# Optimization experiments

Measured on AMD Instinct MI355X. Metric: run time of the kernel, lower is better.

## Reference

```python
import jax, jax.numpy as jnp
import numpy as np

IN_DIM = 1024
QK_DIM = 64
NHEADS = 12
HN_MULT = 4
BATCH = 2
SEQ = 2048
BETA = 1.0 / np.sqrt(QK_DIM)


def setup_inputs() -> dict:
    key = jax.random.key(0)
    kg, kq, kk, kw = jax.random.split(key, 4)
    scale = 1.0 / np.sqrt(IN_DIM)
    g = jax.random.normal(kg, (BATCH, SEQ, IN_DIM), dtype=jnp.float32)
    Wq = jax.random.normal(kq, (NHEADS, QK_DIM, IN_DIM), dtype=jnp.float32) * scale
    Wk = jax.random.normal(kk, (NHEADS, QK_DIM, IN_DIM), dtype=jnp.float32) * scale
    Whn = jax.random.normal(kw, (HN_MULT * IN_DIM, IN_DIM), dtype=jnp.float32) * scale
    return {"g": g, "Wq": Wq, "Wk": Wk, "Whn": Whn}


def reference(g, Wq, Wk, Whn):
    # --- attention energy (Energy Transformer): E = -(1/beta) * sum logsumexp_keys(beta * q.k)
    q = jnp.einsum("bnd,hkd->bhnk", g, Wq)  # [B,H,N,K]
    k = jnp.einsum("bnd,hkd->bhnk", g, Wk)  # [B,H,N,K]
    scores = BETA * jnp.einsum("bhnk,bhmk->bhnm", q, k)  # [B,H,N(query),M(key)]
    e_attn = -(1.0 / BETA) * jnp.sum(jax.nn.logsumexp(scores, axis=-1))
    # --- Hopfield energy: -0.5 * sum(relu(W g)^2)
    h = jnp.einsum("bnd,md->bnm", g, Whn)  # [B,N,4*D]
    e_hn = -0.5 * jnp.sum(jax.nn.relu(h) ** 2)
    return e_attn + e_hn
```

## Files before the change

kernel.cpp:

```cpp
#include <hip/hip_runtime.h>
#include <hip/hip_bf16.h>

typedef __attribute__((ext_vector_type(4))) float f32x4;
typedef __attribute__((ext_vector_type(8))) short bf16x8;
typedef unsigned short u16;
typedef __attribute__((ext_vector_type(4))) u16 u16x4;


#define OFF_GB    ((size_t)0)
#define OFF_WQB   ((size_t)8388608)
#define OFF_WKB   ((size_t)(8388608+1572864))
#define OFF_WHNB  ((size_t)(8388608+2*1572864))
#define OFF_QB    (OFF_WHNB + 8388608)
#define OFF_KB    (OFF_QB + 6291456)
#define OFF_ROWSUM (OFF_KB + 6291456)

__device__ __forceinline__ u16 f2bf(float f) {
  union { float f; unsigned u; } x; x.f = f;
  unsigned u = x.u;
  u += 0x7fffu + ((u >> 16) & 1u);
  return (u16)(u >> 16);
}

__global__ __launch_bounds__(256) void convert_all(
    const float* __restrict__ g, const float* __restrict__ wq,
    const float* __restrict__ wk, const float* __restrict__ whn,
    u16* __restrict__ gB, u16* __restrict__ wqB, u16* __restrict__ wkB, u16* __restrict__ whnB)
{
  const int NG = 1048576;
  const int NW = 196608;
  const int total = NG + 2 * NW + NG;
  for (int i = blockIdx.x * blockDim.x + threadIdx.x; i < total; i += gridDim.x * blockDim.x) {
    const float4* src; u16* dst; int j; float scale = 1.0f;
    if (i < NG)              { src = (const float4*)g;   dst = gB;   j = i; }
    else if (i < NG + NW)    { src = (const float4*)wq;  dst = wqB;  j = i - NG;
                               scale = 0.125f * 1.44269504089f; }
    else if (i < NG + 2*NW)  { src = (const float4*)wk;  dst = wkB;  j = i - NG - NW; }
    else                     { src = (const float4*)whn; dst = whnB; j = i - NG - 2*NW; }
    float4 v = src[j];
    u16x4 o;
    o.x = f2bf(v.x * scale); o.y = f2bf(v.y * scale);
    o.z = f2bf(v.z * scale); o.w = f2bf(v.w * scale);
    *(u16x4*)(dst + (size_t)j * 4) = o;
  }
}

__global__ __launch_bounds__(256) void gemm_bt(
    const u16* __restrict__ A, const u16* __restrict__ B0, const u16* __restrict__ B1,
    u16* __restrict__ C0, u16* __restrict__ C1, int K)
{
  __shared__ u16 lA[128 * 64];
  __shared__ u16 lB[128 * 64];
  const int tid = threadIdx.x;
  const int lane = tid & 63;
  const int w = tid >> 6;
  const int bid = blockIdx.x;
  const int xcd = bid & 7, idx = bid >> 3;
  const int bm = ((xcd >> 1) << 3) + (idx & 7);
  const int bn = (xcd & 1) * 6 + (idx >> 3);

  const u16* Bp; u16* Cp; int bcol0;
  if (bn < 6) { Bp = B0; Cp = C0; bcol0 = bn * 128; }
  else        { Bp = B1; Cp = C1; bcol0 = (bn - 6) * 128; }
  const int arow0 = bm * 128;
  const int wr = w >> 1, wc = w & 1;
  const int l15 = lane & 15, lg = lane >> 4;

  f32x4 acc[4][4];
  const f32x4 zz = {0.f, 0.f, 0.f, 0.f};
#pragma unroll
  for (int m = 0; m < 4; m++)
#pragma unroll
    for (int n = 0; n < 4; n++) acc[m][n] = zz;

#define STAGE(KT) do {                                                                     \
    _Pragma("unroll")                                                                      \
    for (int i = 0; i < 4; i++) {                                                          \
      int rloc = w * 32 + i * 8 + (lane >> 3);                                             \
      int cb   = (((lane & 7) ^ (rloc & 7)) << 4);                                         \
      const char* srcA = (const char*)A + (((size_t)(arow0 + rloc)) * K + (KT) * 64) * 2 + cb; \
      __builtin_amdgcn_global_load_lds((const __attribute__((address_space(1))) void*)srcA, \
          (__attribute__((address_space(3))) void*)((char*)lA + (w * 32 + i * 8) * 128), 16, 0, 0); \
      const char* srcB = (const char*)Bp + (((size_t)(bcol0 + rloc)) * K + (KT) * 64) * 2 + cb; \
      __builtin_amdgcn_global_load_lds((const __attribute__((address_space(1))) void*)srcB, \
          (__attribute__((address_space(3))) void*)((char*)lB + (w * 32 + i * 8) * 128), 16, 0, 0); \
    }                                                                                      \
  } while (0)

  STAGE(0);
  const int nkt = K / 64;
  for (int kt = 0; kt < nkt; ++kt) {
    __syncthreads();
    bf16x8 a0[4], a1[4], b0[4], b1[4];
#pragma unroll
    for (int m = 0; m < 4; m++) {
      int row = wr * 64 + m * 16 + l15;
      const char* base = (const char*)lA + row * 128;
      int sw = (row & 7) << 4;
      a0[m] = *(const bf16x8*)(base + ((lg * 16) ^ sw));
      a1[m] = *(const bf16x8*)(base + ((64 + lg * 16) ^ sw));
    }
#pragma unroll
    for (int n = 0; n < 4; n++) {
      int row = wc * 64 + n * 16 + l15;
      const char* base = (const char*)lB + row * 128;
      int sw = (row & 7) << 4;
      b0[n] = *(const bf16x8*)(base + ((lg * 16) ^ sw));
      b1[n] = *(const bf16x8*)(base + ((64 + lg * 16) ^ sw));
    }
    __syncthreads();
    if (kt + 1 < nkt) STAGE(kt + 1);
#pragma unroll
    for (int m = 0; m < 4; m++)
#pragma unroll
      for (int n = 0; n < 4; n++) {
        acc[m][n] = __builtin_amdgcn_mfma_f32_16x16x32_bf16(a0[m], b0[n], acc[m][n], 0, 0, 0);
        acc[m][n] = __builtin_amdgcn_mfma_f32_16x16x32_bf16(a1[m], b1[n], acc[m][n], 0, 0, 0);
      }
  }
#pragma unroll
  for (int m = 0; m < 4; m++)
#pragma unroll
    for (int n = 0; n < 4; n++)
#pragma unroll
      for (int r = 0; r < 4; r++) {
        int row = arow0 + wr * 64 + m * 16 + lg * 4 + r;
        int col = bcol0 + wc * 64 + n * 16 + l15;
        size_t dst = ((((size_t)(row >> 11) * 12 + (col >> 6)) << 11) + (row & 2047)) * 64 + (col & 63);
        Cp[dst] = f2bf(acc[m][n][r]);
      }
#undef STAGE
}

__global__ __launch_bounds__(512, 2) void hop_gemm8(
    const u16* __restrict__ A, const u16* __restrict__ Bm, float* __restrict__ out)
{
  __shared__ __align__(16) u16 lds[2][2][2][128][64];
  const int tid = threadIdx.x;
  const int lane = tid & 63, w = tid >> 6;
  const int wr = w >> 2, wc = w & 3;
  const int l15 = lane & 15, lg = lane >> 4;
  const int bid = blockIdx.x;
  const int xcd = bid & 7, idx = bid >> 3;
  const int am0 = (((xcd >> 1) << 2) + (idx & 3)) * 256;
  const int bn0 = (((xcd & 1) << 3) + (idx >> 2)) * 256;
  constexpr int nkt = 16;

  f32x4 acc[8][4];
  const f32x4 zz = {0.f, 0.f, 0.f, 0.f};
#pragma unroll
  for (int i = 0; i < 8; i++)
#pragma unroll
    for (int j = 0; j < 4; j++) acc[i][j] = zz;

#define HSTAGE(KT, MAT, H) do {                                                            \
    const u16* s_ = (MAT) ? Bm : A;                                                        \
    int rb_ = ((MAT) ? bn0 : am0) + (H) * 128;                                             \
    char* d0_ = (char*)&lds[(KT) & 1][(MAT)][(H)][0][0];                                   \
    _Pragma("unroll")                                                                      \
    for (int q_ = 0; q_ < 2; q_++) {                                                       \
      int r_ = q_ * 64 + (tid >> 3);                                                       \
      int cb_ = ((tid & 7) * 16) ^ ((r_ & 7) << 4);                                        \
      const char* g_ = (const char*)s_ + (size_t)(rb_ + r_) * 2048 + (KT) * 128 + cb_;     \
      __builtin_amdgcn_global_load_lds((const __attribute__((address_space(1))) void*)g_,  \
          (__attribute__((address_space(3))) void*)(d0_ + q_ * 8192 + tid * 16), 16, 0, 0);\
    }                                                                                      \
  } while (0)

#define LDA_F(DST, P, I, S) do {                                                           \
    int rh_ = ((I) & 3) * 32 + wr * 16 + l15;                                              \
    const char* b_ = (const char*)&lds[(P)][0][(I) >> 2][0][0] + rh_ * 128;                \
    DST = *(const bf16x8*)(b_ + (((S) * 64 + lg * 16) ^ ((rh_ & 7) << 4)));                \
  } while (0)
#define LDB_F(DST, P, J, S) do {                                                           \
    int rh_ = ((J) & 1) * 64 + wc * 16 + l15;                                              \
    const char* b_ = (const char*)&lds[(P)][1][(J) >> 1][0][0] + rh_ * 128;                \
    DST = *(const bf16x8*)(b_ + (((S) * 64 + lg * 16) ^ ((rh_ & 7) << 4)));                \
  } while (0)

  HSTAGE(0, 0, 0); HSTAGE(0, 1, 0); HSTAGE(0, 1, 1); HSTAGE(0, 0, 1);
  HSTAGE(1, 0, 0); HSTAGE(1, 1, 0); HSTAGE(1, 1, 1);
  asm volatile("s_waitcnt vmcnt(6)" ::: "memory");
  __builtin_amdgcn_s_barrier();

  bf16x8 af[4][2], bf[4][2];

#pragma unroll 2
  for (int t = 0; t < nkt; ++t) {
    const int p = t & 1;
#pragma unroll
    for (int m = 0; m < 4; m++) { LDA_F(af[m][0], p, m, 0); LDA_F(af[m][1], p, m, 1); }
#pragma unroll
    for (int n = 0; n < 2; n++) { LDB_F(bf[n][0], p, n, 0); LDB_F(bf[n][1], p, n, 1); }
    if (t + 1 < nkt) HSTAGE(t + 1, 0, 1);
    __builtin_amdgcn_s_barrier();
    __builtin_amdgcn_s_setprio(1);
#pragma unroll
    for (int m = 0; m < 4; m++)
#pragma unroll
      for (int n = 0; n < 2; n++) {
        acc[m][n] = __builtin_amdgcn_mfma_f32_16x16x32_bf16(af[m][0], bf[n][0], acc[m][n], 0, 0, 0);
        acc[m][n] = __builtin_amdgcn_mfma_f32_16x16x32_bf16(af[m][1], bf[n][1], acc[m][n], 0, 0, 0);
      }
    __builtin_amdgcn_s_setprio(0);
    __builtin_amdgcn_s_barrier();
#pragma unroll
    for (int n = 2; n < 4; n++) { LDB_F(bf[n][0], p, n, 0); LDB_F(bf[n][1], p, n, 1); }
    if (t + 2 < nkt) HSTAGE(t + 2, 0, 0);
    __builtin_amdgcn_s_barrier();
    __builtin_amdgcn_s_setprio(1);
#pragma unroll
    for (int m = 0; m < 4; m++)
#pragma unroll
      for (int n = 2; n < 4; n++) {
        acc[m][n] = __builtin_amdgcn_mfma_f32_16x16x32_bf16(af[m][0], bf[n][0], acc[m][n], 0, 0, 0);
        acc[m][n] = __builtin_amdgcn_mfma_f32_16x16x32_bf16(af[m][1], bf[n][1], acc[m][n], 0, 0, 0);
      }
    __builtin_amdgcn_s_setprio(0);
    __builtin_amdgcn_s_barrier();
#pragma unroll
    for (int m = 0; m < 4; m++) { LDA_F(af[m][0], p, m + 4, 0); LDA_F(af[m][1], p, m + 4, 1); }
    if (t + 2 < nkt) HSTAGE(t + 2, 1, 0);
    __builtin_amdgcn_s_barrier();
    __builtin_amdgcn_s_setprio(1);
#pragma unroll
    for (int m = 0; m < 4; m++)
#pragma unroll
      for (int n = 2; n < 4; n++) {
        acc[m + 4][n] = __builtin_amdgcn_mfma_f32_16x16x32_bf16(af[m][0], bf[n][0], acc[m + 4][n], 0, 0, 0);
        acc[m + 4][n] = __builtin_amdgcn_mfma_f32_16x16x32_bf16(af[m][1], bf[n][1], acc[m + 4][n], 0, 0, 0);
      }
    __builtin_amdgcn_s_setprio(0);
    __builtin_amdgcn_s_barrier();
    if (t + 2 < nkt) HSTAGE(t + 2, 1, 1);
    __builtin_amdgcn_s_barrier();
    __builtin_amdgcn_s_setprio(1);
#pragma unroll
    for (int m = 0; m < 4; m++)
#pragma unroll
      for (int n = 0; n < 2; n++) {
        acc[m + 4][n] = __builtin_amdgcn_mfma_f32_16x16x32_bf16(af[m][0], bf[n][0], acc[m + 4][n], 0, 0, 0);
        acc[m + 4][n] = __builtin_amdgcn_mfma_f32_16x16x32_bf16(af[m][1], bf[n][1], acc[m + 4][n], 0, 0, 0);
      }
    __builtin_amdgcn_s_setprio(0);
    if (t < nkt - 2)       asm volatile("s_waitcnt vmcnt(6)" ::: "memory");
    else if (t == nkt - 2) asm volatile("s_waitcnt vmcnt(0)" ::: "memory");
    __builtin_amdgcn_s_barrier();
  }
#undef HSTAGE
#undef LDA_F
#undef LDB_F

  float loc = 0.f;
#pragma unroll
  for (int i = 0; i < 8; i++)
#pragma unroll
    for (int j = 0; j < 4; j++)
#pragma unroll
      for (int r = 0; r < 4; r++) {
        float v = acc[i][j][r];
        loc += (v > 0.f) ? v * v : 0.f;
      }
#pragma unroll
  for (int mask = 32; mask; mask >>= 1) loc += __shfl_xor(loc, mask, 64);
  if (lane == 0) atomicAdd(out, -0.5f * loc);
}

__global__ __launch_bounds__(256) void score_tile(
    const u16* __restrict__ qB, const u16* __restrict__ kB, float* __restrict__ rowsum)
{
  __shared__ __align__(16) u16 qlds[128 * 64];
  __shared__ __align__(16) u16 klds[256 * 64];
  const int z = blockIdx.x, qt = blockIdx.y, kt = blockIdx.z;
  const int tid = threadIdx.x, lane = tid & 63, w = tid >> 6;
  const int l15 = lane & 15, lg = lane >> 4;

#pragma unroll
  for (int i = 0; i < 4; i++) {
    int c = i * 256 + tid;
    int r = c >> 3;
    int cb = ((c & 7) << 4) ^ ((r & 7) << 4);
    const char* src = (const char*)qB + ((size_t)z * 2048 + qt * 128 + r) * 128 + cb;
    __builtin_amdgcn_global_load_lds((const __attribute__((address_space(1))) void*)src,
        (__attribute__((address_space(3))) void*)((char*)qlds + c * 16), 16, 0, 0);
  }
#pragma unroll
  for (int i = 0; i < 8; i++) {
    int c = i * 256 + tid;
    int r = c >> 3;
    int cb = ((c & 7) << 4) ^ ((r & 7) << 4);
    const char* src = (const char*)kB + ((size_t)z * 2048 + kt * 256 + r) * 128 + cb;
    __builtin_amdgcn_global_load_lds((const __attribute__((address_space(1))) void*)src,
        (__attribute__((address_space(3))) void*)((char*)klds + c * 16), 16, 0, 0);
  }
  asm volatile("s_waitcnt vmcnt(0)" ::: "memory");
  __builtin_amdgcn_s_barrier();

  bf16x8 bf[4][2];
#pragma unroll
  for (int n = 0; n < 4; n++) {
    int row = w * 64 + n * 16 + l15;
    const char* base = (const char*)klds + row * 128;
    int sw = (row & 7) << 4;
    bf[n][0] = *(const bf16x8*)(base + ((lg * 16) ^ sw));
    bf[n][1] = *(const bf16x8*)(base + ((64 + lg * 16) ^ sw));
  }

  float rp[8][4];
#pragma unroll
  for (int m = 0; m < 8; m++)
#pragma unroll
    for (int r = 0; r < 4; r++) rp[m][r] = 0.f;

  const f32x4 zz = {0.f, 0.f, 0.f, 0.f};
#pragma unroll
  for (int m = 0; m < 8; m++) {
    int row = m * 16 + l15;
    const char* base = (const char*)qlds + row * 128;
    int sw = (row & 7) << 4;
    bf16x8 a0 = *(const bf16x8*)(base + ((lg * 16) ^ sw));
    bf16x8 a1 = *(const bf16x8*)(base + ((64 + lg * 16) ^ sw));
#pragma unroll
    for (int n = 0; n < 4; n++) {
      f32x4 s = zz;
      s = __builtin_amdgcn_mfma_f32_16x16x32_bf16(a0, bf[n][0], s, 0, 0, 0);
      s = __builtin_amdgcn_mfma_f32_16x16x32_bf16(a1, bf[n][1], s, 0, 0, 0);
      rp[m][0] += __builtin_amdgcn_exp2f(s[0]);
      rp[m][1] += __builtin_amdgcn_exp2f(s[1]);
      rp[m][2] += __builtin_amdgcn_exp2f(s[2]);
      rp[m][3] += __builtin_amdgcn_exp2f(s[3]);
    }
  }

#pragma unroll
  for (int m = 0; m < 8; m++)
#pragma unroll
    for (int r = 0; r < 4; r++) {
#pragma unroll
      for (int mask = 8; mask; mask >>= 1) rp[m][r] += __shfl_xor(rp[m][r], mask, 64);
    }
  if (l15 == 0) {
    float* rs = rowsum + (size_t)z * 2048 + qt * 128;
#pragma unroll
    for (int m = 0; m < 8; m++)
#pragma unroll
      for (int r = 0; r < 4; r++)
        atomicAdd(rs + m * 16 + lg * 4 + r, rp[m][r]);
  }
}

__global__ __launch_bounds__(256) void lse_reduce(
    const float* __restrict__ rowsum, float* __restrict__ out, int n)
{
  float v = 0.f;
  for (int i = blockIdx.x * blockDim.x + threadIdx.x; i < n; i += gridDim.x * blockDim.x)
    v += __builtin_amdgcn_logf(rowsum[i]);
#pragma unroll
  for (int mask = 32; mask; mask >>= 1) v += __shfl_xor(v, mask, 64);
  __shared__ float red[4];
  if ((threadIdx.x & 63) == 0) red[threadIdx.x >> 6] = v;
  __syncthreads();
  if (threadIdx.x == 0) {
    float t = red[0] + red[1] + red[2] + red[3];
    atomicAdd(out, -5.545177444479562f * t);
  }
}

extern "C" void kernel_launch(void* const* d_in, const int* in_sizes, int n_in,
                              void* d_out, int out_size, void* d_ws, size_t ws_size,
                              hipStream_t stream)
{
  const float* g   = (const float*)d_in[0];
  const float* Wq  = (const float*)d_in[1];
  const float* Wk  = (const float*)d_in[2];
  const float* Whn = (const float*)d_in[3];
  float* out = (float*)d_out;
  char* ws = (char*)d_ws;

  u16* gB   = (u16*)(ws + OFF_GB);
  u16* wqB  = (u16*)(ws + OFF_WQB);
  u16* wkB  = (u16*)(ws + OFF_WKB);
  u16* whnB = (u16*)(ws + OFF_WHNB);
  u16* qB   = (u16*)(ws + OFF_QB);
  u16* kB   = (u16*)(ws + OFF_KB);
  float* rowsum = (float*)(ws + OFF_ROWSUM);

  (void)hipMemsetAsync(out, 0, sizeof(float), stream);
  (void)hipMemsetAsync(rowsum, 0, 49152 * sizeof(float), stream);

  convert_all<<<2048, 256, 0, stream>>>(g, Wq, Wk, Whn, gB, wqB, wkB, whnB);
  gemm_bt<<<384, 256, 0, stream>>>(gB, wqB, wkB, qB, kB, 1024);
  hop_gemm8<<<256, 512, 0, stream>>>(gB, whnB, out);
  score_tile<<<dim3(24, 16, 8), 256, 0, stream>>>(qB, kB, rowsum);
  lse_reduce<<<96, 256, 0, stream>>>(rowsum, out, 49152);
}
```

Baseline: 198.7 us.

## Halve QK projection GEMM tile height and replace rowsum atomics with partial buffers

The Q/K projection GEMM now uses 64x128 tiles instead of 128x128, which doubles the grid to 768 blocks so the machine fills more evenly. The staging loads are reindexed to match. The score kernel now writes per-key-tile partial row sums to separate slots instead of issuing atomicAdds, and lse_reduce sums the 32 partials before taking the log. This also removes the rowsum memset. The trade-off is a larger workspace footprint and more global reads in the reduce.

```diff
diff --git a/kernel.cpp b/kernel.cpp
--- a/kernel.cpp
+++ b/kernel.cpp
@@ -49,41 +49,48 @@
     const u16* __restrict__ A, const u16* __restrict__ B0, const u16* __restrict__ B1,
     u16* __restrict__ C0, u16* __restrict__ C1, int K)
 {
-  __shared__ u16 lA[128 * 64];
-  __shared__ u16 lB[128 * 64];
+  __shared__ __align__(16) u16 lA[64 * 64];
+  __shared__ __align__(16) u16 lB[128 * 64];
   const int tid = threadIdx.x;
   const int lane = tid & 63;
   const int w = tid >> 6;
   const int bid = blockIdx.x;
   const int xcd = bid & 7, idx = bid >> 3;
-  const int bm = ((xcd >> 1) << 3) + (idx & 7);
-  const int bn = (xcd & 1) * 6 + (idx >> 3);
+  const int bm = xcd * 8 + (idx & 7);
+  const int bn = idx >> 3;
 
   const u16* Bp; u16* Cp; int bcol0;
   if (bn < 6) { Bp = B0; Cp = C0; bcol0 = bn * 128; }
   else        { Bp = B1; Cp = C1; bcol0 = (bn - 6) * 128; }
-  const int arow0 = bm * 128;
+  const int arow0 = bm * 64;
   const int wr = w >> 1, wc = w & 1;
   const int l15 = lane & 15, lg = lane >> 4;
 
-  f32x4 acc[4][4];
+  f32x4 acc[2][4];
   const f32x4 zz = {0.f, 0.f, 0.f, 0.f};
 #pragma unroll
-  for (int m = 0; m < 4; m++)
+  for (int m = 0; m < 2; m++)
 #pragma unroll
     for (int n = 0; n < 4; n++) acc[m][n] = zz;
 
 #define STAGE(KT) do {                                                                     \
     _Pragma("unroll")                                                                      \
+    for (int i = 0; i < 2; i++) {                                                          \
+      int c = i * 256 + tid;                                                               \
+      int r = c >> 3;                                                                      \
+      int cb = (((c & 7) ^ (r & 7)) << 4);                                                 \
+      const char* src = (const char*)A + (((size_t)(arow0 + r)) * K + (KT) * 64) * 2 + cb; \
+      __builtin_amdgcn_global_load_lds((const __attribute__((address_space(1))) void*)src, \
+          (__attribute__((address_space(3))) void*)((char*)lA + c * 16), 16, 0, 0);        \
+    }                                                                                      \
+    _Pragma("unroll")                                                                      \
     for (int i = 0; i < 4; i++) {                                                          \
-      int rloc = w * 32 + i * 8 + (lane >> 3);                                             \
-      int cb   = (((lane & 7) ^ (rloc & 7)) << 4);                                         \
-      const char* srcA = (const char*)A + (((size_t)(arow0 + rloc)) * K + (KT) * 64) * 2 + cb; \
-      __builtin_amdgcn_global_load_lds((const __attribute__((address_space(1))) void*)srcA, \
-          (__attribute__((address_space(3))) void*)((char*)lA + (w * 32 + i * 8) * 128), 16, 0, 0); \
-      const char* srcB = (const char*)Bp + (((size_t)(bcol0 + rloc)) * K + (KT) * 64) * 2 + cb; \
-      __builtin_amdgcn_global_load_lds((const __attribute__((address_space(1))) void*)srcB, \
-          (__attribute__((address_space(3))) void*)((char*)lB + (w * 32 + i * 8) * 128), 16, 0, 0); \
+      int c = i * 256 + tid;                                                               \
+      int r = c >> 3;                                                                      \
+      int cb = (((c & 7) ^ (r & 7)) << 4);                                                 \
+      const char* src = (const char*)Bp + (((size_t)(bcol0 + r)) * K + (KT) * 64) * 2 + cb;\
+      __builtin_amdgcn_global_load_lds((const __attribute__((address_space(1))) void*)src, \
+          (__attribute__((address_space(3))) void*)((char*)lB + c * 16), 16, 0, 0);        \
     }                                                                                      \
   } while (0)
 
@@ -91,10 +98,10 @@
   const int nkt = K / 64;
   for (int kt = 0; kt < nkt; ++kt) {
     __syncthreads();
-    bf16x8 a0[4], a1[4], b0[4], b1[4];
-#pragma unroll
-    for (int m = 0; m < 4; m++) {
-      int row = wr * 64 + m * 16 + l15;
+    bf16x8 a0[2], a1[2], b0[4], b1[4];
+#pragma unroll
+    for (int m = 0; m < 2; m++) {
+      int row = wr * 32 + m * 16 + l15;
       const char* base = (const char*)lA + row * 128;
       int sw = (row & 7) << 4;
       a0[m] = *(const bf16x8*)(base + ((lg * 16) ^ sw));
@@ -111,7 +118,7 @@
     __syncthreads();
     if (kt + 1 < nkt) STAGE(kt + 1);
 #pragma unroll
-    for (int m = 0; m < 4; m++)
+    for (int m = 0; m < 2; m++)
 #pragma unroll
       for (int n = 0; n < 4; n++) {
         acc[m][n] = __builtin_amdgcn_mfma_f32_16x16x32_bf16(a0[m], b0[n], acc[m][n], 0, 0, 0);
@@ -119,12 +126,12 @@
       }
   }
 #pragma unroll
-  for (int m = 0; m < 4; m++)
+  for (int m = 0; m < 2; m++)
 #pragma unroll
     for (int n = 0; n < 4; n++)
 #pragma unroll
       for (int r = 0; r < 4; r++) {
-        int row = arow0 + wr * 64 + m * 16 + lg * 4 + r;
+        int row = arow0 + wr * 32 + m * 16 + lg * 4 + r;
         int col = bcol0 + wc * 64 + n * 16 + l15;
         size_t dst = ((((size_t)(row >> 11) * 12 + (col >> 6)) << 11) + (row & 2047)) * 64 + (col & 63);
         Cp[dst] = f2bf(acc[m][n][r]);
@@ -340,12 +347,12 @@
       for (int mask = 8; mask; mask >>= 1) rp[m][r] += __shfl_xor(rp[m][r], mask, 64);
     }
   if (l15 == 0) {
-    float* rs = rowsum + (size_t)z * 2048 + qt * 128;
+    float* rs = rowsum + ((size_t)(kt * 4 + w) * 24 + z) * 2048 + qt * 128;
 #pragma unroll
     for (int m = 0; m < 8; m++)
 #pragma unroll
       for (int r = 0; r < 4; r++)
-        atomicAdd(rs + m * 16 + lg * 4 + r, rp[m][r]);
+        rs[m * 16 + lg * 4 + r] = rp[m][r];
   }
 }
 
@@ -353,8 +360,12 @@
     const float* __restrict__ rowsum, float* __restrict__ out, int n)
 {
   float v = 0.f;
-  for (int i = blockIdx.x * blockDim.x + threadIdx.x; i < n; i += gridDim.x * blockDim.x)
-    v += __builtin_amdgcn_logf(rowsum[i]);
+  for (int i = blockIdx.x * blockDim.x + threadIdx.x; i < n; i += gridDim.x * blockDim.x) {
+    float s = 0.f;
+#pragma unroll
+    for (int kt = 0; kt < 32; kt++) s += rowsum[(size_t)kt * 49152 + i];
+    v += __builtin_amdgcn_logf(s);
+  }
 #pragma unroll
   for (int mask = 32; mask; mask >>= 1) v += __shfl_xor(v, mask, 64);
   __shared__ float red[4];
@@ -386,10 +397,9 @@
   float* rowsum = (float*)(ws + OFF_ROWSUM);
 
   (void)hipMemsetAsync(out, 0, sizeof(float), stream);
-  (void)hipMemsetAsync(rowsum, 0, 49152 * sizeof(float), stream);
 
   convert_all<<<2048, 256, 0, stream>>>(g, Wq, Wk, Whn, gB, wqB, wkB, whnB);
-  gemm_bt<<<384, 256, 0, stream>>>(gB, wqB, wkB, qB, kB, 1024);
+  gemm_bt<<<768, 256, 0, stream>>>(gB, wqB, wkB, qB, kB, 1024);
   hop_gemm8<<<256, 512, 0, stream>>>(gB, whnB, out);
   score_tile<<<dim3(24, 16, 8), 256, 0, stream>>>(qB, kB, rowsum);
   lse_reduce<<<96, 256, 0, stream>>>(rowsum, out, 49152);
```

Result: faster. 187.5 us (-5.6%).
